# Performance work log

Hardware: AMD Instinct MI355X
Metric: run time of the kernel (lower is better)

Reference implementation:

```python
import jax, jax.numpy as jnp
import numpy as np

B, S, HID = 1, 2048, 4096
NH, NKV, HD = 32, 8, 128
GROUPS = NH // NKV
SCALING = HD ** -0.5


def approx_matmul(a, b):
    # BaselineApproxMatmulFP16: matmul performed in fp16 precision
    return jnp.matmul(a.astype(jnp.float16), b.astype(jnp.float16)).astype(a.dtype)


def rotate_half(x):
    x1, x2 = jnp.split(x, 2, axis=-1)
    return jnp.concatenate([-x2, x1], axis=-1)


def setup_inputs() -> dict:
    key = jax.random.key(0)
    ks = jax.random.split(key, 6)
    hidden_states = jax.random.normal(ks[0], (B, S, HID), jnp.float32)
    # Proper RoPE tables (HF llama convention: freqs duplicated across halves)
    inv_freq = 1.0 / (10000.0 ** (jnp.arange(0, HD, 2, dtype=jnp.float32) / HD))
    t = jnp.arange(S, dtype=jnp.float32)
    freqs = jnp.outer(t, inv_freq)                      # [S, HD/2]
    emb = jnp.concatenate([freqs, freqs], axis=-1)      # [S, HD]
    cos = jnp.cos(emb)[None]                            # [B, S, HD]
    sin = jnp.sin(emb)[None]
    # Additive causal mask [B,1,S,S]
    causal = jnp.triu(jnp.full((S, S), -1e9, jnp.float32), k=1)[None, None]
    scale = 0.02
    wq = jax.random.normal(ks[1], (HID, NH * HD), jnp.float32) * scale
    wk = jax.random.normal(ks[2], (HID, NKV * HD), jnp.float32) * scale
    wv = jax.random.normal(ks[3], (HID, NKV * HD), jnp.float32) * scale
    wo = jax.random.normal(ks[4], (NH * HD, HID), jnp.float32) * scale
    return {"hidden_states": hidden_states, "cos": cos, "sin": sin,
            "attn_mask": causal, "wq": wq, "wk": wk, "wv": wv, "wo": wo}


def reference(hidden_states, cos, sin, attn_mask, wq, wk, wv, wo):
    x = hidden_states
    # projections -> [B, heads, S, HD]
    q = (x @ wq).reshape(B, S, NH, HD).transpose(0, 2, 1, 3)
    k = (x @ wk).reshape(B, S, NKV, HD).transpose(0, 2, 1, 3)
    v = (x @ wv).reshape(B, S, NKV, HD).transpose(0, 2, 1, 3)
    # RoPE
    c = cos[:, None]  # [B,1,S,HD]
    s = sin[:, None]
    q = q * c + rotate_half(q) * s
    k = k * c + rotate_half(k) * s
    # repeat_kv (GQA): [B,NKV,S,HD] -> [B,NH,S,HD]
    k = jnp.repeat(k, GROUPS, axis=1)
    v = jnp.repeat(v, GROUPS, axis=1)
    # eager attention with fp16 approx matmul
    attn = approx_matmul(q, k.transpose(0, 1, 3, 2)) * SCALING  # [B,NH,S,S]
    attn = attn + attn_mask
    attn = jax.nn.softmax(attn.astype(jnp.float32), axis=-1).astype(q.dtype)
    out = approx_matmul(attn, v)                                # [B,NH,S,HD]
    out = out.transpose(0, 2, 1, 3).reshape(B, S, NH * HD)
    return out @ wo
```

## Files before the change

kernel.cpp:

```cpp
#include <hip/hip_runtime.h>
#include <hip/hip_bf16.h>
#include <hip/hip_fp16.h>

typedef _Float16 half8 __attribute__((ext_vector_type(8)));
typedef _Float16 half4 __attribute__((ext_vector_type(4)));
typedef float f32x4 __attribute__((ext_vector_type(4)));
typedef unsigned int u32;

#define S_LEN 2048
#define HID_DIM 4096
#define N_HEADS 32
#define N_KV 8
#define HEAD_DIM 128
#define SCALE_QK 0.08838834764831845f

__device__ __forceinline__ void async16(void* lds, const void* gptr) {
  __builtin_amdgcn_global_load_lds(
      (const __attribute__((address_space(1))) u32*)gptr,
      (__attribute__((address_space(3))) u32*)lds, 16, 0, 0);
}

__global__ void conv_f32_f16(const float* __restrict__ src, _Float16* __restrict__ dst, int n4) {
  int i = blockIdx.x * 256 + threadIdx.x;
  if (i < n4) {
    float4 v = ((const float4*)src)[i];
    half4 h;
    h[0] = (_Float16)v.x; h[1] = (_Float16)v.y; h[2] = (_Float16)v.z; h[3] = (_Float16)v.w;
    ((half4*)dst)[i] = h;
  }
}

__global__ void transpose_f32_f16(const float* __restrict__ src, _Float16* __restrict__ dst,
                                  int R, int C) {
  __shared__ _Float16 tile[64][33];
  int bx = blockIdx.x;
  int by = blockIdx.y;
  int x = threadIdx.x, y = threadIdx.y;
#pragma unroll
  for (int k = 0; k < 8; k++)
    tile[y + 8 * k][x] = (_Float16)src[(long)(by * 64 + y + 8 * k) * C + bx * 32 + x];
  __syncthreads();
  int tid = y * 32 + x;
  int r = tid & 63;
  int cb = tid >> 6;
#pragma unroll
  for (int w = 0; w < 8; w++) {
    int c = w * 4 + cb;
    dst[(long)(bx * 32 + c) * R + by * 64 + r] = tile[r][c];
  }
}

template <int NHEADS>
__global__ void rope_tiled(_Float16* __restrict__ t, const float* __restrict__ cosb,
                           const float* __restrict__ sinb) {
  int idx = blockIdx.x * 256 + threadIdx.x;
  int slo = idx & 15;
  int d8 = (idx >> 4) & 7;
  int h = (idx >> 7) % NHEADS;
  int s16 = idx / (128 * NHEADS);
  int s = s16 * 16 + slo;
  int d0 = d8 * 8;
  long c0 = (long)(h * 128 + s16) * 4;
  long base = (c0 + (d0 >> 5)) * 512 + ((d0 >> 3) & 3) * 128 + slo * 8;
  half8 a = *(half8*)(t + base);
  half8 b = *(half8*)(t + base + 1024);
  const float* cp = cosb + s * 128 + d0;
  const float* sp = sinb + s * 128 + d0;
  half8 olo, ohi;
#pragma unroll
  for (int j = 0; j < 8; j++) {
    float c = cp[j], sn = sp[j];
    float av = (float)a[j], bv = (float)b[j];
    olo[j] = (_Float16)(av * c - bv * sn);
    ohi[j] = (_Float16)(bv * c + av * sn);
  }
  *(half8*)(t + base) = olo;
  *(half8*)(t + base + 1024) = ohi;
}

__global__ __launch_bounds__(256, 3) void gemm_qkv(
    const _Float16* __restrict__ A, const _Float16* __restrict__ BtQ,
    const _Float16* __restrict__ BtKV, _Float16* __restrict__ Qt,
    _Float16* __restrict__ Kt, _Float16* __restrict__ Vt) {
  __shared__ _Float16 As[128 * 64];
  __shared__ _Float16 Bs[128 * 64];
  const int K = 4096;
  const int tid = threadIdx.x, lane = tid & 63, wid = tid >> 6;
  const int row0 = blockIdx.y * 128;
  const int col0 = blockIdx.x * 128;
  const int wm = wid >> 1, wn = wid & 1;
  const int lr = lane & 15, lg = lane >> 4;

  const _Float16* bbase = (col0 < 4096) ? (BtQ + (long)col0 * K)
                                        : (BtKV + (long)(col0 - 4096) * K);
  const int scol = ((lane & 7) ^ ((lane >> 3) & 7)) * 8;
  const _Float16* aptr = A + (long)(row0 + wid * 32 + (lane >> 3)) * K + scol;
  const _Float16* bptr = bbase + (long)(wid * 32 + (lane >> 3)) * K + scol;
  _Float16* alds = As + (wid * 4) * 512;
  _Float16* blds = Bs + (wid * 4) * 512;

  f32x4 acc[4][4] = {};
  for (int k0 = 0; k0 < K; k0 += 64) {
#pragma unroll
    for (int j = 0; j < 4; j++) {
      async16(alds + j * 512, aptr + k0 + (long)j * 8 * K);
      async16(blds + j * 512, bptr + k0 + (long)j * 8 * K);
    }
    __syncthreads();
    half8 a[2][4], b[2][4];
#pragma unroll
    for (int kk = 0; kk < 2; kk++)
#pragma unroll
      for (int mf = 0; mf < 4; mf++) {
        a[kk][mf] = *(const half8*)&As[(wm * 64 + mf * 16 + lr) * 64 +
                                       (((kk * 4 + lg) ^ (lr & 7)) * 8)];
        b[kk][mf] = *(const half8*)&Bs[(wn * 64 + mf * 16 + lr) * 64 +
                                       (((kk * 4 + lg) ^ (lr & 7)) * 8)];
      }
#pragma unroll
    for (int kk = 0; kk < 2; kk++)
#pragma unroll
      for (int mf = 0; mf < 4; mf++)
#pragma unroll
        for (int nf = 0; nf < 4; nf++)
          acc[mf][nf] =
              __builtin_amdgcn_mfma_f32_16x16x32_f16(a[kk][mf], b[kk][nf], acc[mf][nf], 0, 0, 0);
    __syncthreads();
  }

#pragma unroll
  for (int mf = 0; mf < 4; mf++) {
#pragma unroll
    for (int nf = 0; nf < 4; nf++) {
      int rbase = row0 + wm * 64 + mf * 16 + lg * 4;
      int col = col0 + wn * 64 + nf * 16 + lr;
      if (col0 < 4096) {
        int h = col >> 7, d = col & 127;
        long off = ((long)((h * 128 + (rbase >> 4)) * 4 + (d >> 5))) * 512 +
                   ((d >> 3) & 3) * 128 + (rbase & 15) * 8 + (d & 7);
#pragma unroll
        for (int i = 0; i < 4; i++) Qt[off + i * 8] = (_Float16)acc[mf][nf][i];
      } else if (col0 < 5120) {
        int gc = col - 4096;
        int g = gc >> 7, d = gc & 127;
        long off = ((long)((g * 128 + (rbase >> 4)) * 4 + (d >> 5))) * 512 +
                   ((d >> 3) & 3) * 128 + (rbase & 15) * 8 + (d & 7);
#pragma unroll
        for (int i = 0; i < 4; i++) Kt[off + i * 8] = (_Float16)acc[mf][nf][i];
      } else {
        int gc = col - 5120;
        int gq = gc >> 7, d = gc & 127;
        int dt = d >> 4, lrr = d & 15;
        int kvb = rbase >> 5, lgv = (rbase >> 3) & 3, j = rbase & 7;
        half4 v;
#pragma unroll
        for (int i = 0; i < 4; i++) v[i] = (_Float16)acc[mf][nf][i];
        long off = ((long)(gq * 64 + kvb) * 8 + dt) * 512 + (lgv * 16 + lrr) * 8 + j;
        *(half4*)&Vt[off] = v;
      }
    }
  }
}

__global__ __launch_bounds__(256, 3) void gemm_out(
    const _Float16* __restrict__ A, const _Float16* __restrict__ Bt,
    float* __restrict__ C) {
  __shared__ _Float16 As[128 * 64];
  __shared__ _Float16 Bs[128 * 64];
  const int K = 4096;
  const int tid = threadIdx.x, lane = tid & 63, wid = tid >> 6;
  const int row0 = blockIdx.y * 128;
  const int col0 = blockIdx.x * 128;
  const int wm = wid >> 1, wn = wid & 1;
  const int lr = lane & 15, lg = lane >> 4;

  const int scol = ((lane & 7) ^ ((lane >> 3) & 7)) * 8;
  const _Float16* aptr = A + (long)(row0 + wid * 32 + (lane >> 3)) * K + scol;
  const _Float16* bptr = Bt + (long)(col0 + wid * 32 + (lane >> 3)) * K + scol;
  _Float16* alds = As + (wid * 4) * 512;
  _Float16* blds = Bs + (wid * 4) * 512;

  f32x4 acc[4][4] = {};
  for (int k0 = 0; k0 < K; k0 += 64) {
#pragma unroll
    for (int j = 0; j < 4; j++) {
      async16(alds + j * 512, aptr + k0 + (long)j * 8 * K);
      async16(blds + j * 512, bptr + k0 + (long)j * 8 * K);
    }
    __syncthreads();
    half8 a[2][4], b[2][4];
#pragma unroll
    for (int kk = 0; kk < 2; kk++)
#pragma unroll
      for (int mf = 0; mf < 4; mf++) {
        a[kk][mf] = *(const half8*)&As[(wm * 64 + mf * 16 + lr) * 64 +
                                       (((kk * 4 + lg) ^ (lr & 7)) * 8)];
        b[kk][mf] = *(const half8*)&Bs[(wn * 64 + mf * 16 + lr) * 64 +
                                       (((kk * 4 + lg) ^ (lr & 7)) * 8)];
      }
#pragma unroll
    for (int kk = 0; kk < 2; kk++)
#pragma unroll
      for (int mf = 0; mf < 4; mf++)
#pragma unroll
        for (int nf = 0; nf < 4; nf++)
          acc[mf][nf] =
              __builtin_amdgcn_mfma_f32_16x16x32_f16(a[kk][mf], b[kk][nf], acc[mf][nf], 0, 0, 0);
    __syncthreads();
  }
#pragma unroll
  for (int mf = 0; mf < 4; mf++)
#pragma unroll
    for (int nf = 0; nf < 4; nf++) {
      int rbase = row0 + wm * 64 + mf * 16 + lg * 4;
      int col = col0 + wn * 64 + nf * 16 + lr;
#pragma unroll
      for (int i = 0; i < 4; i++)
        C[(long)(rbase + i) * 4096 + col] = acc[mf][nf][i];
    }
}

__global__ __launch_bounds__(256, 3) void attn_kernel(
    const _Float16* __restrict__ Qt, const _Float16* __restrict__ Kt,
    const _Float16* __restrict__ Vt, _Float16* __restrict__ O) {
  __shared__ _Float16 Klds[2][4096];
  __shared__ _Float16 Vlds[2][4096];
  __shared__ _Float16 P_lds[4][512];
  const int tid = threadIdx.x;
  const int lane = tid & 63;
  const int wid = tid >> 6;
  const int bid = blockIdx.x;
  const int g = bid & 7;
  const int qidx = bid >> 3;
  const int qt16 = (qidx < 64) ? (2 * qidx) : (2 * (127 - qidx) + 1);
  const int h = g * 4 + wid;
  const int qrow0 = qt16 * 16;
  const int ntiles = (qrow0 + 47) >> 5;
  const int lr = lane & 15;
  const int lg = lane >> 4;

  half8 qf[4];
  {
    const _Float16* qp = Qt + ((long)(h * 128 + qt16) * 4) * 512 + lane * 8;
#pragma unroll
    for (int t = 0; t < 4; t++) qf[t] = *(const half8*)(qp + t * 512);
  }

  const _Float16* kgb = Kt + (long)g * 128 * 2048 + lane * 8;
  const _Float16* vgb = Vt + (long)g * 64 * 4096 + lane * 8;

  {
    async16(&Klds[0][(2 * wid) * 512], kgb + (2 * wid) * 512);
    async16(&Klds[0][(2 * wid + 1) * 512], kgb + (2 * wid + 1) * 512);
    async16(&Vlds[0][(2 * wid) * 512], vgb + (2 * wid) * 512);
    async16(&Vlds[0][(2 * wid + 1) * 512], vgb + (2 * wid + 1) * 512);
  }
  __syncthreads();

  f32x4 oacc[8] = {};
  float mrow[4] = {-1e30f, -1e30f, -1e30f, -1e30f};
  float lsum[4] = {0.f, 0.f, 0.f, 0.f};

  for (int t = 0; t < ntiles; t++) {
    const int kb = t * 32;
    const int cur = t & 1;
    if (t + 1 < ntiles) {
      const _Float16* ks = kgb + (long)(t + 1) * 4096;
      const _Float16* vs = vgb + (long)(t + 1) * 4096;
      async16(&Klds[cur ^ 1][(2 * wid) * 512], ks + (2 * wid) * 512);
      async16(&Klds[cur ^ 1][(2 * wid + 1) * 512], ks + (2 * wid + 1) * 512);
      async16(&Vlds[cur ^ 1][(2 * wid) * 512], vs + (2 * wid) * 512);
      async16(&Vlds[cur ^ 1][(2 * wid + 1) * 512], vs + (2 * wid + 1) * 512);
    }

    half8 kf[8];
#pragma unroll
    for (int c = 0; c < 8; c++)
      kf[c] = *(const half8*)&Klds[cur][c * 512 + lane * 8];
    half8 vf[8];
#pragma unroll
    for (int dt = 0; dt < 8; dt++)
      vf[dt] = *(const half8*)&Vlds[cur][dt * 512 + lane * 8];

    f32x4 sacc[2] = {};
#pragma unroll
    for (int s = 0; s < 2; s++)
#pragma unroll
      for (int t2 = 0; t2 < 4; t2++)
        sacc[s] = __builtin_amdgcn_mfma_f32_16x16x32_f16(qf[t2], kf[s * 4 + t2], sacc[s], 0, 0, 0);

    float mx[4];
    bool grow = false;
#pragma unroll
    for (int i = 0; i < 4; i++) {
      int qrow = qrow0 + lg * 4 + i;
      float s0 = sacc[0][i] * SCALE_QK;
      float s1 = sacc[1][i] * SCALE_QK;
      if (kb + lr > qrow) s0 = -1e30f;
      if (kb + 16 + lr > qrow) s1 = -1e30f;
      sacc[0][i] = s0; sacc[1][i] = s1;
      mx[i] = fmaxf(s0, s1);
      grow |= (mx[i] > mrow[i] + 4.0f);
    }
    if (__any((int)grow)) {
#pragma unroll
      for (int i = 0; i < 4; i++) {
        float m = mx[i];
        m = fmaxf(m, __shfl_xor(m, 1));
        m = fmaxf(m, __shfl_xor(m, 2));
        m = fmaxf(m, __shfl_xor(m, 4));
        m = fmaxf(m, __shfl_xor(m, 8));
        float mn = fmaxf(mrow[i], m);
        float scl = __expf(mrow[i] - mn);
        mrow[i] = mn;
        lsum[i] *= scl;
#pragma unroll
        for (int dt = 0; dt < 8; dt++) oacc[dt][i] *= scl;
      }
    }
    float p[2][4];
#pragma unroll
    for (int i = 0; i < 4; i++) {
      p[0][i] = __expf(sacc[0][i] - mrow[i]);
      p[1][i] = __expf(sacc[1][i] - mrow[i]);
      lsum[i] += p[0][i] + p[1][i];
    }

#pragma unroll
    for (int sub = 0; sub < 2; sub++)
#pragma unroll
      for (int i = 0; i < 4; i++)
        P_lds[wid][(lg * 4 + i) * 32 + sub * 16 + lr] = (_Float16)p[sub][i];
    half8 pa = *(const half8*)&P_lds[wid][lr * 32 + lg * 8];

#pragma unroll
    for (int dt = 0; dt < 8; dt++)
      oacc[dt] = __builtin_amdgcn_mfma_f32_16x16x32_f16(pa, vf[dt], oacc[dt], 0, 0, 0);

    __syncthreads();
  }

#pragma unroll
  for (int i = 0; i < 4; i++) {
    float t2 = lsum[i];
    t2 += __shfl_xor(t2, 1);
    t2 += __shfl_xor(t2, 2);
    t2 += __shfl_xor(t2, 4);
    t2 += __shfl_xor(t2, 8);
    lsum[i] = t2;
  }
#pragma unroll
  for (int dt = 0; dt < 8; dt++) {
#pragma unroll
    for (int i = 0; i < 4; i++) {
      float o = oacc[dt][i] / lsum[i];
      O[(long)(qrow0 + lg * 4 + i) * HID_DIM + h * HEAD_DIM + dt * 16 + lr] = (_Float16)o;
    }
  }
}

extern "C" void kernel_launch(void* const* d_in, const int* in_sizes, int n_in,
                              void* d_out, int out_size, void* d_ws, size_t ws_size,
                              hipStream_t stream) {
  const float* x    = (const float*)d_in[0];
  const float* cosb = (const float*)d_in[1];
  const float* sinb = (const float*)d_in[2];
  const float* wq = (const float*)d_in[4];
  const float* wk = (const float*)d_in[5];
  const float* wv = (const float*)d_in[6];
  const float* wo = (const float*)d_in[7];
  float* out = (float*)d_out;

  char* ws = (char*)d_ws;
  _Float16* Xh    = (_Float16*)(ws);
  _Float16* Oattn = Xh;
  _Float16* Qt    = (_Float16*)(ws + (size_t)(16 << 20));
  _Float16* Kt    = (_Float16*)(ws + (size_t)(32 << 20));
  _Float16* Vt    = (_Float16*)(ws + (size_t)(36 << 20));
  _Float16* WqT   = (_Float16*)(ws + (size_t)(40 << 20));
  _Float16* WoT   = WqT;
  _Float16* WkvT  = (_Float16*)d_out;

  dim3 b256(256);
  dim3 tb(32, 8);

  conv_f32_f16<<<dim3(S_LEN * HID_DIM / 4 / 256), b256, 0, stream>>>(x, Xh, S_LEN * HID_DIM / 4);

  transpose_f32_f16<<<dim3(4096 / 32, 4096 / 64), tb, 0, stream>>>(wq, WqT, 4096, 4096);
  transpose_f32_f16<<<dim3(1024 / 32, 4096 / 64), tb, 0, stream>>>(wk, WkvT, 4096, 1024);
  transpose_f32_f16<<<dim3(1024 / 32, 4096 / 64), tb, 0, stream>>>(wv, WkvT + (size_t)1024 * 4096, 4096, 1024);

  gemm_qkv<<<dim3(6144 / 128, S_LEN / 128), b256, 0, stream>>>(Xh, WqT, WkvT, Qt, Kt, Vt);

  rope_tiled<N_HEADS><<<dim3(N_HEADS * 16384 / 256), b256, 0, stream>>>(Qt, cosb, sinb);
  rope_tiled<N_KV><<<dim3(N_KV * 16384 / 256), b256, 0, stream>>>(Kt, cosb, sinb);

  attn_kernel<<<dim3(1024), b256, 0, stream>>>(Qt, Kt, Vt, Oattn);

  transpose_f32_f16<<<dim3(4096 / 32, 4096 / 64), tb, 0, stream>>>(wo, WoT, 4096, 4096);
  gemm_out<<<dim3(4096 / 128, S_LEN / 128), b256, 0, stream>>>(Oattn, WoT, out);
}
```

Measured before the change: 327.7 us.

## Fuse Q RoPE into attention, vectorize weight transpose and input conversion

The Q RoPE pass moves into the attention kernel, which now rotates the Q fragments in registers after loading them. This removes the separate Q rope kernel and its read/write of the Q buffer. The weight transpose now uses 64x64 tiles with float4 loads and half8 stores, and the fp32-to-fp16 conversion handles eight elements per thread. In exchange, the attention prologue gains extra global loads of the cos/sin tables, and the transpose uses a larger shared-memory tile.

```diff
diff --git a/kernel.cpp b/kernel.cpp
--- a/kernel.cpp
+++ b/kernel.cpp
@@ -20,33 +20,44 @@
       (__attribute__((address_space(3))) u32*)lds, 16, 0, 0);
 }
 
-__global__ void conv_f32_f16(const float* __restrict__ src, _Float16* __restrict__ dst, int n4) {
+__global__ void conv_f32_f16(const float* __restrict__ src, _Float16* __restrict__ dst, int n8) {
   int i = blockIdx.x * 256 + threadIdx.x;
-  if (i < n4) {
-    float4 v = ((const float4*)src)[i];
-    half4 h;
-    h[0] = (_Float16)v.x; h[1] = (_Float16)v.y; h[2] = (_Float16)v.z; h[3] = (_Float16)v.w;
-    ((half4*)dst)[i] = h;
+  if (i < n8) {
+    float4 a = ((const float4*)src)[2 * i];
+    float4 b = ((const float4*)src)[2 * i + 1];
+    half8 h;
+    h[0] = (_Float16)a.x; h[1] = (_Float16)a.y; h[2] = (_Float16)a.z; h[3] = (_Float16)a.w;
+    h[4] = (_Float16)b.x; h[5] = (_Float16)b.y; h[6] = (_Float16)b.z; h[7] = (_Float16)b.w;
+    ((half8*)dst)[i] = h;
   }
 }
 
 __global__ void transpose_f32_f16(const float* __restrict__ src, _Float16* __restrict__ dst,
                                   int R, int C) {
-  __shared__ _Float16 tile[64][33];
-  int bx = blockIdx.x;
-  int by = blockIdx.y;
-  int x = threadIdx.x, y = threadIdx.y;
-#pragma unroll
-  for (int k = 0; k < 8; k++)
-    tile[y + 8 * k][x] = (_Float16)src[(long)(by * 64 + y + 8 * k) * C + bx * 32 + x];
+  __shared__ float tile[64][73];
+  const int t = threadIdx.x;
+  const int bx = blockIdx.x;
+  const int by = blockIdx.y;
+  {
+    const int c4 = (t & 15) * 4;
+    const int r0 = t >> 4;
+#pragma unroll
+    for (int i = 0; i < 4; i++) {
+      int r = r0 + 16 * i;
+      float4 v = *(const float4*)&src[(long)(by * 64 + r) * C + bx * 64 + c4];
+      tile[r][c4] = v.x; tile[r][c4 + 1] = v.y; tile[r][c4 + 2] = v.z; tile[r][c4 + 3] = v.w;
+    }
+  }
   __syncthreads();
-  int tid = y * 32 + x;
-  int r = tid & 63;
-  int cb = tid >> 6;
-#pragma unroll
-  for (int w = 0; w < 8; w++) {
-    int c = w * 4 + cb;
-    dst[(long)(bx * 32 + c) * R + by * 64 + r] = tile[r][c];
+  const int kc = t & 7;
+  const int n0 = t >> 3;
+#pragma unroll
+  for (int p = 0; p < 2; p++) {
+    int n = n0 + 32 * p;
+    half8 o;
+#pragma unroll
+    for (int j = 0; j < 8; j++) o[j] = (_Float16)tile[kc * 8 + j][n];
+    *(half8*)&dst[(long)(bx * 64 + n) * R + by * 64 + kc * 8] = o;
   }
 }
 
@@ -222,7 +233,8 @@
 
 __global__ __launch_bounds__(256, 3) void attn_kernel(
     const _Float16* __restrict__ Qt, const _Float16* __restrict__ Kt,
-    const _Float16* __restrict__ Vt, _Float16* __restrict__ O) {
+    const _Float16* __restrict__ Vt, _Float16* __restrict__ O,
+    const float* __restrict__ cosb, const float* __restrict__ sinb) {
   __shared__ _Float16 Klds[2][4096];
   __shared__ _Float16 Vlds[2][4096];
   __shared__ _Float16 P_lds[4][512];
@@ -244,6 +256,19 @@
     const _Float16* qp = Qt + ((long)(h * 128 + qt16) * 4) * 512 + lane * 8;
 #pragma unroll
     for (int t = 0; t < 4; t++) qf[t] = *(const half8*)(qp + t * 512);
+    int s = qrow0 + lr;
+#pragma unroll
+    for (int t = 0; t < 2; t++) {
+      const float* cp = cosb + s * 128 + t * 32 + lg * 8;
+      const float* sp = sinb + s * 128 + t * 32 + lg * 8;
+#pragma unroll
+      for (int j = 0; j < 8; j++) {
+        float c = cp[j], sn = sp[j];
+        float lo = (float)qf[t][j], hi = (float)qf[t + 2][j];
+        qf[t][j]     = (_Float16)(lo * c - hi * sn);
+        qf[t + 2][j] = (_Float16)(hi * c + lo * sn);
+      }
+    }
   }
 
   const _Float16* kgb = Kt + (long)g * 128 * 2048 + lane * 8;
@@ -382,21 +407,19 @@
   _Float16* WkvT  = (_Float16*)d_out;
 
   dim3 b256(256);
-  dim3 tb(32, 8);
-
-  conv_f32_f16<<<dim3(S_LEN * HID_DIM / 4 / 256), b256, 0, stream>>>(x, Xh, S_LEN * HID_DIM / 4);
-
-  transpose_f32_f16<<<dim3(4096 / 32, 4096 / 64), tb, 0, stream>>>(wq, WqT, 4096, 4096);
-  transpose_f32_f16<<<dim3(1024 / 32, 4096 / 64), tb, 0, stream>>>(wk, WkvT, 4096, 1024);
-  transpose_f32_f16<<<dim3(1024 / 32, 4096 / 64), tb, 0, stream>>>(wv, WkvT + (size_t)1024 * 4096, 4096, 1024);
+
+  conv_f32_f16<<<dim3(S_LEN * HID_DIM / 8 / 256), b256, 0, stream>>>(x, Xh, S_LEN * HID_DIM / 8);
+
+  transpose_f32_f16<<<dim3(4096 / 64, 4096 / 64), b256, 0, stream>>>(wq, WqT, 4096, 4096);
+  transpose_f32_f16<<<dim3(1024 / 64, 4096 / 64), b256, 0, stream>>>(wk, WkvT, 4096, 1024);
+  transpose_f32_f16<<<dim3(1024 / 64, 4096 / 64), b256, 0, stream>>>(wv, WkvT + (size_t)1024 * 4096, 4096, 1024);
 
   gemm_qkv<<<dim3(6144 / 128, S_LEN / 128), b256, 0, stream>>>(Xh, WqT, WkvT, Qt, Kt, Vt);
 
-  rope_tiled<N_HEADS><<<dim3(N_HEADS * 16384 / 256), b256, 0, stream>>>(Qt, cosb, sinb);
   rope_tiled<N_KV><<<dim3(N_KV * 16384 / 256), b256, 0, stream>>>(Kt, cosb, sinb);
 
-  attn_kernel<<<dim3(1024), b256, 0, stream>>>(Qt, Kt, Vt, Oattn);
-
-  transpose_f32_f16<<<dim3(4096 / 32, 4096 / 64), tb, 0, stream>>>(wo, WoT, 4096, 4096);
+  attn_kernel<<<dim3(1024), b256, 0, stream>>>(Qt, Kt, Vt, Oattn, cosb, sinb);
+
+  transpose_f32_f16<<<dim3(4096 / 64, 4096 / 64), b256, 0, stream>>>(wo, WoT, 4096, 4096);
   gemm_out<<<dim3(4096 / 128, S_LEN / 128), b256, 0, stream>>>(Oattn, WoT, out);
 }
```

Measured after the change: 320.1 us. 2.3% less time.
